# Kernel optimization log

Measured on AMD Instinct MI355X. Metric: run time of the kernel, lower is better.

## Reference

```python
import jax, jax.numpy as jnp
import numpy as np

B, N, D, FH, FW, C = 1, 6, 118, 32, 88, 80
IH, IW = 256, 704
XB = (-54.0, 54.0, 0.3); YB = (-54.0, 54.0, 0.3); ZB = (-10.0, 10.0, 20.0); DB = (1.0, 60.0, 0.5)
NX, NY, NZ = 360, 360, 1


def _frustum():
    # [D, fH, fW, 3] of (pixel_x, pixel_y, depth)
    ds = jnp.broadcast_to(jnp.arange(DB[0], DB[1], DB[2], dtype=jnp.float32)[:, None, None], (D, FH, FW))
    xs = jnp.broadcast_to(jnp.linspace(0.0, IW - 1, FW, dtype=jnp.float32)[None, None, :], (D, FH, FW))
    ys = jnp.broadcast_to(jnp.linspace(0.0, IH - 1, FH, dtype=jnp.float32)[None, :, None], (D, FH, FW))
    return jnp.stack((xs, ys, ds), -1)


def setup_inputs() -> dict:
    key = jax.random.key(0)
    k = jax.random.split(key, 6)
    cam_feats = jax.random.normal(k[0], (B, N, D, FH, FW, C), dtype=jnp.float32)
    eye4 = jnp.eye(4, dtype=jnp.float32)
    # camera->ego: near-orthonormal rotation (I + small noise) + translation; invertibility not needed for rots
    c2e = jnp.broadcast_to(eye4, (B, N, 4, 4))
    c2e = c2e.at[..., :3, :3].add(0.05 * jax.random.normal(k[1], (B, N, 3, 3), dtype=jnp.float32))
    c2e = c2e.at[..., :3, 3].set(jax.random.uniform(k[2], (B, N, 3), dtype=jnp.float32, minval=-1.0, maxval=1.0))
    # pinhole intrinsics (focal 560, principal point at image center) -> well-conditioned inverse
    intr = jnp.broadcast_to(eye4, (B, N, 4, 4))
    intr = intr.at[..., 0, 0].set(560.0).at[..., 1, 1].set(560.0)
    intr = intr.at[..., 0, 2].set(IW / 2.0).at[..., 1, 2].set(IH / 2.0)
    # image augmentation matrix: near identity + small pixel shift (must be invertible)
    aug = jnp.broadcast_to(eye4, (B, N, 4, 4))
    aug = aug.at[..., :3, :3].add(0.01 * jax.random.normal(k[3], (B, N, 3, 3), dtype=jnp.float32))
    aug = aug.at[..., :2, 3].set(jax.random.uniform(k[4], (B, N, 2), dtype=jnp.float32, minval=-2.0, maxval=2.0))
    l2e = jnp.broadcast_to(eye4, (B, 4, 4))
    laug = jnp.broadcast_to(eye4, (B, 4, 4))
    laug = laug.at[..., :3, :3].add(0.01 * jax.random.normal(k[5], (B, 3, 3), dtype=jnp.float32))
    return dict(cam_feats=cam_feats, camera2ego=c2e, lidar2ego=l2e,
                camera_intrinsics=intr, img_aug_matrix=aug, lidar_aug_matrix=laug)


def _geometry(camera2ego, lidar2ego, camera_intrinsics, img_aug_matrix, lidar_aug_matrix):
    rots = camera2ego[..., :3, :3]; trans = camera2ego[..., :3, 3]
    intrins = camera_intrinsics[..., :3, :3]
    post_rots = img_aug_matrix[..., :3, :3]; post_trans = img_aug_matrix[..., :3, 3]
    l2e_r = lidar2ego[..., :3, :3]; l2e_t = lidar2ego[..., :3, 3]
    er = lidar_aug_matrix[..., :3, :3]; et = lidar_aug_matrix[..., :3, 3]
    pts = _frustum()[None, None] - post_trans[:, :, None, None, None, :]       # [B,N,D,H,W,3]
    pts = jnp.einsum('bnij,bndhwj->bndhwi', jnp.linalg.inv(post_rots), pts)
    pts = jnp.concatenate([pts[..., :2] * pts[..., 2:3], pts[..., 2:3]], -1)   # un-normalize pixels by depth
    combine = rots @ jnp.linalg.inv(intrins)
    pts = jnp.einsum('bnij,bndhwj->bndhwi', combine, pts) + trans[:, :, None, None, None, :]
    pts = pts - l2e_t[:, None, None, None, None, :]
    pts = jnp.einsum('bij,bndhwj->bndhwi', jnp.linalg.inv(l2e_r), pts)
    pts = jnp.einsum('bij,bndhwj->bndhwi', er, pts) + et[:, None, None, None, None, :]
    return pts


def _bev_pool(geom, x):
    dx = jnp.array([XB[2], YB[2], ZB[2]], dtype=jnp.float32)
    bx = jnp.array([XB[0] + XB[2] / 2.0, YB[0] + YB[2] / 2.0, ZB[0] + ZB[2] / 2.0], dtype=jnp.float32)
    Nprime = B * N * D * FH * FW
    feats = x.reshape(Nprime, C)
    # torch .long() truncates toward zero; jnp int cast matches
    coords = ((geom - (bx - dx / 2.0)) / dx).reshape(Nprime, 3).astype(jnp.int32)
    batch_ix = jnp.repeat(jnp.arange(B, dtype=jnp.int32), Nprime // B)
    kept = ((coords[:, 0] >= 0) & (coords[:, 0] < NX) &
            (coords[:, 1] >= 0) & (coords[:, 1] < NY) &
            (coords[:, 2] >= 0) & (coords[:, 2] < NZ))
    cc = jnp.where(kept[:, None], coords, 0)
    idx = ((batch_ix * NZ + cc[:, 2]) * NX + cc[:, 0]) * NY + cc[:, 1]
    feats = jnp.where(kept[:, None], feats, 0.0)
    pooled = jax.ops.segment_sum(feats, idx, num_segments=B * NZ * NX * NY)    # [B*Z*X*Y, C]
    pooled = pooled.reshape(B, NZ, NX, NY, C)
    # torch: final[B,C,Z,X,Y] -> cat(unbind(dim=2), dim=1) == [B, Z*C, X, Y]
    return jnp.transpose(pooled, (0, 1, 4, 2, 3)).reshape(B, NZ * C, NX, NY)


def reference(cam_feats, camera2ego, lidar2ego, camera_intrinsics, img_aug_matrix, lidar_aug_matrix):
    geom = _geometry(camera2ego, lidar2ego, camera_intrinsics, img_aug_matrix, lidar_aug_matrix)
    return _bev_pool(geom, cam_feats)
```

## Files before the change

### kernel.cpp

```cpp
#include <hip/hip_runtime.h>

#define NCAM 6
#define DD 118
#define FHH 32
#define FWW 88
#define CC 80
#define NXV 360
#define NYV 360
#define NVOX (NXV * NYV)
#define PTS_PER_CAM (DD * FHH * FWW)
#define NPTS (NCAM * PTS_PER_CAM)
#define BLK 256
#define NPT_BLOCKS (NPTS / BLK)
#define SCAN_BLOCKS ((NVOX + 255) / 256)
#define SEG 64
#define MAX_SEGS 196608

#define WS_P      0
#define WS_CNT    1536
#define WS_NSEG   (WS_CNT + NVOX * 4)
#define WS_CURSOR (WS_NSEG + 16)
#define WS_BSUM   (WS_CURSOR + NVOX * 4)
#define WS_SEGS   (WS_BSUM + 2048)
#define WS_IDX    (WS_SEGS + MAX_SEGS * 16)

__device__ __forceinline__ void inv3x3d(const double* m, double* inv) {
    double c00 = m[4] * m[8] - m[5] * m[7];
    double c01 = m[3] * m[8] - m[5] * m[6];
    double c02 = m[3] * m[7] - m[4] * m[6];
    double det = m[0] * c00 - m[1] * c01 + m[2] * c02;
    double id  = 1.0 / det;
    inv[0] =  c00 * id;
    inv[1] = (m[2] * m[7] - m[1] * m[8]) * id;
    inv[2] = (m[1] * m[5] - m[2] * m[4]) * id;
    inv[3] = -c01 * id;
    inv[4] = (m[0] * m[8] - m[2] * m[6]) * id;
    inv[5] = (m[2] * m[3] - m[0] * m[5]) * id;
    inv[6] =  c02 * id;
    inv[7] = (m[1] * m[6] - m[0] * m[7]) * id;
    inv[8] = (m[0] * m[4] - m[1] * m[3]) * id;
}

__global__ void precomp_kernel(const float* __restrict__ c2e,
                               const float* __restrict__ l2e,
                               const float* __restrict__ intr,
                               const float* __restrict__ aug,
                               const float* __restrict__ laug,
                               float* __restrict__ P) {
    int n = threadIdx.x;
    if (n >= NCAM) return;
    double rots[9], intrins[9], post[9], l2er[9], er[9];
    double trans[3], ptrans[3], l2et[3], et[3];
    for (int i = 0; i < 3; i++) {
        for (int j = 0; j < 3; j++) {
            rots[i * 3 + j]    = c2e[n * 16 + i * 4 + j];
            intrins[i * 3 + j] = intr[n * 16 + i * 4 + j];
            post[i * 3 + j]    = aug[n * 16 + i * 4 + j];
            l2er[i * 3 + j]    = l2e[i * 4 + j];
            er[i * 3 + j]      = laug[i * 4 + j];
        }
        trans[i]  = c2e[n * 16 + i * 4 + 3];
        ptrans[i] = aug[n * 16 + i * 4 + 3];
        l2et[i]   = l2e[i * 4 + 3];
        et[i]     = laug[i * 4 + 3];
    }
    double A[9], IC[9], L[9], Cm[9];
    inv3x3d(post, A);
    inv3x3d(intrins, IC);
    inv3x3d(l2er, L);
    for (int i = 0; i < 3; i++)
        for (int j = 0; j < 3; j++)
            Cm[i * 3 + j] = rots[i * 3 + 0] * IC[0 + j] +
                            rots[i * 3 + 1] * IC[3 + j] +
                            rots[i * 3 + 2] * IC[6 + j];
    float* p = P + n * 48;
    for (int k = 0; k < 9; k++) p[k]      = (float)A[k];
    for (int k = 0; k < 3; k++) p[9 + k]  = (float)ptrans[k];
    for (int k = 0; k < 9; k++) p[12 + k] = (float)Cm[k];
    for (int k = 0; k < 3; k++) p[21 + k] = (float)trans[k];
    for (int k = 0; k < 3; k++) p[24 + k] = (float)l2et[k];
    for (int k = 0; k < 9; k++) p[27 + k] = (float)L[k];
    for (int k = 0; k < 9; k++) p[36 + k] = (float)er[k];
    for (int k = 0; k < 3; k++) p[45 + k] = (float)et[k];
}

__device__ __forceinline__ int point_voxel(const float* __restrict__ P, int gid) {
    int cam   = gid / PTS_PER_CAM;
    int local = gid - cam * PTS_PER_CAM;
    int d   = local / (FHH * FWW);
    int rem = local - d * (FHH * FWW);
    int h   = rem / FWW;
    int w   = rem - h * FWW;
    const float* p = P + cam * 48;

    float fx = (float)((double)w * (703.0 / 87.0));
    float fy = (float)((double)h * (255.0 / 31.0));
    float fd = 1.0f + 0.5f * (float)d;

    float vx = fx - p[9], vy = fy - p[10], vz = fd - p[11];
    float qx = p[0] * vx + p[1] * vy + p[2] * vz;
    float qy = p[3] * vx + p[4] * vy + p[5] * vz;
    float qz = p[6] * vx + p[7] * vy + p[8] * vz;
    float px = qx * qz, py = qy * qz, pz = qz;
    float rx = p[12] * px + p[13] * py + p[14] * pz + p[21];
    float ry = p[15] * px + p[16] * py + p[17] * pz + p[22];
    float rz = p[18] * px + p[19] * py + p[20] * pz + p[23];
    rx -= p[24]; ry -= p[25]; rz -= p[26];
    float sx = p[27] * rx + p[28] * ry + p[29] * rz;
    float sy = p[30] * rx + p[31] * ry + p[32] * rz;
    float sz = p[33] * rx + p[34] * ry + p[35] * rz;
    float gx = p[36] * sx + p[37] * sy + p[38] * sz + p[45];
    float gy = p[39] * sx + p[40] * sy + p[41] * sz + p[46];
    float gz = p[42] * sx + p[43] * sy + p[44] * sz + p[47];

    const float offx = (-54.0f + 0.15f) - 0.15f;
    const float offy = (-54.0f + 0.15f) - 0.15f;
    const float offz = -10.0f;
    int cx = (int)((gx - offx) / 0.3f);
    int cy = (int)((gy - offy) / 0.3f);
    int cz = (int)((gz - offz) / 20.0f);
    bool kept = (cx >= 0) & (cx < NXV) & (cy >= 0) & (cy < NYV) &
                (cz >= 0) & (cz < 1);
    return kept ? (cx * NYV + cy) : -1;
}

__global__ __launch_bounds__(BLK) void geom_count_kernel(
        const float* __restrict__ P, int* __restrict__ cnt) {
    int gid = blockIdx.x * BLK + threadIdx.x;
    int lane = threadIdx.x & 63;
    int vox = point_voxel(P, gid);
    unsigned long long active = __ballot(vox >= 0);
    while (active) {
        int leader = __ffsll((long long)active) - 1;
        int lvox = __shfl(vox, leader);
        unsigned long long match = __ballot(vox == lvox) & active;
        if (lane == leader) atomicAdd(&cnt[lvox], __popcll(match));
        active &= ~match;
    }
}

__global__ __launch_bounds__(256) void scan1_kernel(
        const int* __restrict__ cnt, int* __restrict__ cursor,
        int* __restrict__ bsum) {
    __shared__ int sh[256];
    int tid = threadIdx.x;
    int i = blockIdx.x * 256 + tid;
    int v = (i < NVOX) ? cnt[i] : 0;
    sh[tid] = v;
    __syncthreads();
    for (int o = 1; o < 256; o <<= 1) {
        int t = (tid >= o) ? sh[tid - o] : 0;
        __syncthreads();
        sh[tid] += t;
        __syncthreads();
    }
    int incl = sh[tid];
    if (i < NVOX) cursor[i] = incl - v;
    if (tid == 255) bsum[blockIdx.x] = incl;
}

__global__ __launch_bounds__(512) void scan2_kernel(int* __restrict__ bsum) {
    __shared__ int sh[512];
    int tid = threadIdx.x;
    int v = (tid < SCAN_BLOCKS) ? bsum[tid] : 0;
    sh[tid] = v;
    __syncthreads();
    for (int o = 1; o < 512; o <<= 1) {
        int t = (tid >= o) ? sh[tid - o] : 0;
        __syncthreads();
        sh[tid] += t;
        __syncthreads();
    }
    if (tid < SCAN_BLOCKS) bsum[tid] = sh[tid] - v;
}

__global__ __launch_bounds__(256) void scan3_kernel(
        int* __restrict__ cursor, const int* __restrict__ bsum) {
    int i = blockIdx.x * 256 + threadIdx.x;
    if (i < NVOX) cursor[i] += bsum[blockIdx.x];
}

__global__ __launch_bounds__(256) void buildsegs_kernel(
        const int* __restrict__ cnt, const int* __restrict__ cursor,
        int* __restrict__ nseg, int4* __restrict__ segs) {
    int v = blockIdx.x * 256 + threadIdx.x;
    if (v >= NVOX) return;
    int c = cnt[v];
    if (c == 0) return;
    int ns = (c + SEG - 1) / SEG;
    int base = atomicAdd(nseg, ns);
    int off0 = cursor[v];
    int hv = (c > SEG) ? 1 : 0;
    for (int k = 0; k < ns; k++) {
        if (base + k < MAX_SEGS) {
            int len = min(SEG, c - k * SEG);
            segs[base + k] = make_int4(v, off0 + k * SEG, len, hv);
        }
    }
}

__global__ __launch_bounds__(BLK) void fill_kernel(
        const float* __restrict__ P, int* __restrict__ cursor,
        int* __restrict__ idx) {
    int gid = blockIdx.x * BLK + threadIdx.x;
    int lane = threadIdx.x & 63;
    int vox = point_voxel(P, gid);
    unsigned long long lt = (lane == 0) ? 0ull : (~0ull >> (64 - lane));
    unsigned long long active = __ballot(vox >= 0);
    while (active) {
        int leader = __ffsll((long long)active) - 1;
        int lvox = __shfl(vox, leader);
        unsigned long long match = __ballot(vox == lvox) & active;
        int base = 0;
        if (lane == leader) base = atomicAdd(&cursor[lvox], __popcll(match));
        base = __shfl(base, leader);
        if ((match >> lane) & 1ull) {
            int rank = __popcll(match & lt);
            idx[base + rank] = gid;
        }
        active &= ~match;
    }
}

__global__ __launch_bounds__(256) void gather_kernel(
        const float* __restrict__ feats,
        const int* __restrict__ nseg,
        const int4* __restrict__ segs,
        const int* __restrict__ idx,
        float* __restrict__ out) {
    int lane = threadIdx.x & 63;
    int wid = (blockIdx.x * 256 + threadIdx.x) >> 6;
    int nwaves = gridDim.x * 4;
    int n = *nseg;
    if (n > MAX_SEGS) n = MAX_SEGS;

    for (int s = wid; s < n; s += nwaves) {
        int4 sg = segs[s];
        int vox = sg.x, start = sg.y, len = sg.z, heavy = sg.w;
        int pt_l = (lane < len) ? idx[start + lane] : 0;
        float a0 = 0.f, a1 = 0.f;
        int j = 0;
        for (; j + 4 <= len; j += 4) {
            int p0 = __shfl(pt_l, j);
            int p1 = __shfl(pt_l, j + 1);
            int p2 = __shfl(pt_l, j + 2);
            int p3 = __shfl(pt_l, j + 3);
            const float* r0 = feats + (size_t)p0 * CC;
            const float* r1 = feats + (size_t)p1 * CC;
            const float* r2 = feats + (size_t)p2 * CC;
            const float* r3 = feats + (size_t)p3 * CC;
            float x0 = r0[lane], x1 = r1[lane], x2 = r2[lane], x3 = r3[lane];
            float y0 = 0.f, y1 = 0.f, y2 = 0.f, y3 = 0.f;
            if (lane < 16) {
                y0 = r0[64 + lane]; y1 = r1[64 + lane];
                y2 = r2[64 + lane]; y3 = r3[64 + lane];
            }
            a0 += (x0 + x1) + (x2 + x3);
            a1 += (y0 + y1) + (y2 + y3);
        }
        for (; j < len; ++j) {
            int p0 = __shfl(pt_l, j);
            const float* r0 = feats + (size_t)p0 * CC;
            a0 += r0[lane];
            if (lane < 16) a1 += r0[64 + lane];
        }
        float* o0 = out + (size_t)lane * NVOX + vox;
        float* o1 = out + (size_t)(64 + lane) * NVOX + vox;
        if (heavy) {
            atomicAdd(o0, a0);
            if (lane < 16) atomicAdd(o1, a1);
        } else {
            *o0 = a0;
            if (lane < 16) *o1 = a1;
        }
    }
}

extern "C" void kernel_launch(void* const* d_in, const int* in_sizes, int n_in,
                              void* d_out, int out_size, void* d_ws, size_t ws_size,
                              hipStream_t stream) {
    const float* feats = (const float*)d_in[0];
    const float* c2e   = (const float*)d_in[1];
    const float* l2e   = (const float*)d_in[2];
    const float* intr  = (const float*)d_in[3];
    const float* aug   = (const float*)d_in[4];
    const float* laug  = (const float*)d_in[5];
    float* out = (float*)d_out;

    char* ws = (char*)d_ws;
    float* P      = (float*)(ws + WS_P);
    int*   cnt    = (int*)(ws + WS_CNT);
    int*   nseg   = (int*)(ws + WS_NSEG);
    int*   cursor = (int*)(ws + WS_CURSOR);
    int*   bsum   = (int*)(ws + WS_BSUM);
    int4*  segs   = (int4*)(ws + WS_SEGS);
    int*   idx    = (int*)(ws + WS_IDX);

    hipMemsetAsync(cnt, 0, NVOX * 4 + 16, stream);
    hipMemsetAsync(out, 0, (size_t)out_size * sizeof(float), stream);
    precomp_kernel<<<1, 64, 0, stream>>>(c2e, l2e, intr, aug, laug, P);
    geom_count_kernel<<<NPT_BLOCKS, BLK, 0, stream>>>(P, cnt);
    scan1_kernel<<<SCAN_BLOCKS, 256, 0, stream>>>(cnt, cursor, bsum);
    scan2_kernel<<<1, 512, 0, stream>>>(bsum);
    scan3_kernel<<<SCAN_BLOCKS, 256, 0, stream>>>(cursor, bsum);
    buildsegs_kernel<<<SCAN_BLOCKS, 256, 0, stream>>>(cnt, cursor, nseg, segs);
    fill_kernel<<<NPT_BLOCKS, BLK, 0, stream>>>(P, cursor, idx);
    gather_kernel<<<4096, 256, 0, stream>>>(feats, nseg, segs, idx, out);
}
```

Before: 912.3 us.

## Record per-point voxel rank in count pass and drop recompute in fill

The count kernel now does a per-point atomic on the voxel counter and stores the voxel id and the returned rank packed into one word per point. The fill kernel reads this word and writes its index directly, with no second geometry computation and no atomics. The separate scan-offset kernel is folded into the segment builder. The cost is an extra per-point buffer and uncoalesced contended atomics instead of wave-aggregated ones. A 15-bit rank field also risks overflow if a voxel receives more than 32767 points.

```diff
diff --git a/kernel.cpp b/kernel.cpp
--- a/kernel.cpp
+++ b/kernel.cpp
@@ -23,6 +23,9 @@
 #define WS_BSUM   (WS_CURSOR + NVOX * 4)
 #define WS_SEGS   (WS_BSUM + 2048)
 #define WS_IDX    (WS_SEGS + MAX_SEGS * 16)
+#define WS_VOXR   (WS_IDX + NPTS * 4)
+
+#define VOXR_EMPTY 0xFFFFFFFFu
 
 __device__ __forceinline__ void inv3x3d(const double* m, double* inv) {
     double c00 = m[4] * m[8] - m[5] * m[7];
@@ -124,19 +127,17 @@
     return kept ? (cx * NYV + cy) : -1;
 }
 
-__global__ __launch_bounds__(BLK) void geom_count_kernel(
-        const float* __restrict__ P, int* __restrict__ cnt) {
+__global__ __launch_bounds__(BLK) void geom_vox_kernel(
+        const float* __restrict__ P, int* __restrict__ cnt,
+        unsigned* __restrict__ voxr) {
     int gid = blockIdx.x * BLK + threadIdx.x;
-    int lane = threadIdx.x & 63;
     int vox = point_voxel(P, gid);
-    unsigned long long active = __ballot(vox >= 0);
-    while (active) {
-        int leader = __ffsll((long long)active) - 1;
-        int lvox = __shfl(vox, leader);
-        unsigned long long match = __ballot(vox == lvox) & active;
-        if (lane == leader) atomicAdd(&cnt[lvox], __popcll(match));
-        active &= ~match;
-    }
+    unsigned pr = VOXR_EMPTY;
+    if (vox >= 0) {
+        int rank = atomicAdd(&cnt[vox], 1);
+        pr = (unsigned)vox | ((unsigned)rank << 17);
+    }
+    voxr[gid] = pr;
 }
 
 __global__ __launch_bounds__(256) void scan1_kernel(
@@ -174,22 +175,18 @@
     if (tid < SCAN_BLOCKS) bsum[tid] = sh[tid] - v;
 }
 
-__global__ __launch_bounds__(256) void scan3_kernel(
-        int* __restrict__ cursor, const int* __restrict__ bsum) {
-    int i = blockIdx.x * 256 + threadIdx.x;
-    if (i < NVOX) cursor[i] += bsum[blockIdx.x];
-}
-
 __global__ __launch_bounds__(256) void buildsegs_kernel(
-        const int* __restrict__ cnt, const int* __restrict__ cursor,
+        const int* __restrict__ cnt, int* __restrict__ cursor,
+        const int* __restrict__ bsum,
         int* __restrict__ nseg, int4* __restrict__ segs) {
     int v = blockIdx.x * 256 + threadIdx.x;
     if (v >= NVOX) return;
+    int off0 = cursor[v] + bsum[blockIdx.x];
+    cursor[v] = off0;
     int c = cnt[v];
     if (c == 0) return;
     int ns = (c + SEG - 1) / SEG;
     int base = atomicAdd(nseg, ns);
-    int off0 = cursor[v];
     int hv = (c > SEG) ? 1 : 0;
     for (int k = 0; k < ns; k++) {
         if (base + k < MAX_SEGS) {
@@ -200,26 +197,14 @@
 }
 
 __global__ __launch_bounds__(BLK) void fill_kernel(
-        const float* __restrict__ P, int* __restrict__ cursor,
+        const unsigned* __restrict__ voxr, const int* __restrict__ cursor,
         int* __restrict__ idx) {
     int gid = blockIdx.x * BLK + threadIdx.x;
-    int lane = threadIdx.x & 63;
-    int vox = point_voxel(P, gid);
-    unsigned long long lt = (lane == 0) ? 0ull : (~0ull >> (64 - lane));
-    unsigned long long active = __ballot(vox >= 0);
-    while (active) {
-        int leader = __ffsll((long long)active) - 1;
-        int lvox = __shfl(vox, leader);
-        unsigned long long match = __ballot(vox == lvox) & active;
-        int base = 0;
-        if (lane == leader) base = atomicAdd(&cursor[lvox], __popcll(match));
-        base = __shfl(base, leader);
-        if ((match >> lane) & 1ull) {
-            int rank = __popcll(match & lt);
-            idx[base + rank] = gid;
-        }
-        active &= ~match;
-    }
+    unsigned pr = voxr[gid];
+    if (pr == VOXR_EMPTY) return;
+    int vox  = (int)(pr & 0x1FFFFu);
+    int rank = (int)(pr >> 17);
+    idx[cursor[vox] + rank] = gid;
 }
 
 __global__ __launch_bounds__(256) void gather_kernel(
@@ -288,22 +273,22 @@
     float* out = (float*)d_out;
 
     char* ws = (char*)d_ws;
-    float* P      = (float*)(ws + WS_P);
-    int*   cnt    = (int*)(ws + WS_CNT);
-    int*   nseg   = (int*)(ws + WS_NSEG);
-    int*   cursor = (int*)(ws + WS_CURSOR);
-    int*   bsum   = (int*)(ws + WS_BSUM);
-    int4*  segs   = (int4*)(ws + WS_SEGS);
-    int*   idx    = (int*)(ws + WS_IDX);
+    float*    P      = (float*)(ws + WS_P);
+    int*      cnt    = (int*)(ws + WS_CNT);
+    int*      nseg   = (int*)(ws + WS_NSEG);
+    int*      cursor = (int*)(ws + WS_CURSOR);
+    int*      bsum   = (int*)(ws + WS_BSUM);
+    int4*     segs   = (int4*)(ws + WS_SEGS);
+    int*      idx    = (int*)(ws + WS_IDX);
+    unsigned* voxr   = (unsigned*)(ws + WS_VOXR);
 
     hipMemsetAsync(cnt, 0, NVOX * 4 + 16, stream);
     hipMemsetAsync(out, 0, (size_t)out_size * sizeof(float), stream);
     precomp_kernel<<<1, 64, 0, stream>>>(c2e, l2e, intr, aug, laug, P);
-    geom_count_kernel<<<NPT_BLOCKS, BLK, 0, stream>>>(P, cnt);
+    geom_vox_kernel<<<NPT_BLOCKS, BLK, 0, stream>>>(P, cnt, voxr);
     scan1_kernel<<<SCAN_BLOCKS, 256, 0, stream>>>(cnt, cursor, bsum);
     scan2_kernel<<<1, 512, 0, stream>>>(bsum);
-    scan3_kernel<<<SCAN_BLOCKS, 256, 0, stream>>>(cursor, bsum);
-    buildsegs_kernel<<<SCAN_BLOCKS, 256, 0, stream>>>(cnt, cursor, nseg, segs);
-    fill_kernel<<<NPT_BLOCKS, BLK, 0, stream>>>(P, cursor, idx);
+    buildsegs_kernel<<<SCAN_BLOCKS, 256, 0, stream>>>(cnt, cursor, bsum, nseg, segs);
+    fill_kernel<<<NPT_BLOCKS, BLK, 0, stream>>>(voxr, cursor, idx);
     gather_kernel<<<4096, 256, 0, stream>>>(feats, nseg, segs, idx, out);
 }
```

Result: slower. 1.186 ms (+30.0%).
